# Performance work log

Measured on AMD Instinct MI355X. Metric: run time of the kernel, lower is better.

Reference implementation:

```python
import jax, jax.numpy as jnp
import numpy as np

S, D, BN, GH, AH, FCH = 18, 512, 32, 128, 16, 512


def setup_inputs() -> dict:
    key = jax.random.key(0)
    ks = jax.random.split(key, 20)
    B = 8192
    sc = 0.05
    inp = {
        "local_styles": jax.random.normal(ks[0], (B, S, D), jnp.float32),
        "global_styles": jax.random.normal(ks[1], (B, S, D), jnp.float32),
        "target_ages": jax.random.uniform(ks[2], (B,), jnp.float32),
        # per-style bottleneck MLPs (512->32->32), stacked over styles
        "bn_w1": jax.random.normal(ks[3], (S, D, BN), jnp.float32) * sc,
        "bn_b1": jnp.zeros((S, BN), jnp.float32),
        "bn_w2": jax.random.normal(ks[4], (S, BN, BN), jnp.float32) * sc,
        "bn_b2": jnp.zeros((S, BN), jnp.float32),
        # global mlp (18*32 -> 128 -> 128)
        "gm_w1": jax.random.normal(ks[5], (S * BN, GH), jnp.float32) * sc,
        "gm_b1": jnp.zeros((GH,), jnp.float32),
        "gm_w2": jax.random.normal(ks[6], (GH, GH), jnp.float32) * sc,
        "gm_b2": jnp.zeros((GH,), jnp.float32),
        # age mlp (1 -> 16 -> 16)
        "age_w1": jax.random.normal(ks[7], (1, AH), jnp.float32) * sc,
        "age_b1": jnp.zeros((AH,), jnp.float32),
        "age_w2": jax.random.normal(ks[8], (AH, AH), jnp.float32) * sc,
        "age_b2": jnp.zeros((AH,), jnp.float32),
        # per-style fc MLPs (128+16+512 -> 512 -> 512), stacked over styles
        "fc_w1": jax.random.normal(ks[9], (S, GH + AH + D, FCH), jnp.float32) * sc,
        "fc_b1": jnp.zeros((S, FCH), jnp.float32),
        "fc_w2": jax.random.normal(ks[10], (S, FCH, D), jnp.float32) * sc,
        "fc_b2": jnp.zeros((S, D), jnp.float32),
    }
    return inp


def reference(local_styles, global_styles, target_ages,
              bn_w1, bn_b1, bn_w2, bn_b2,
              gm_w1, gm_b1, gm_w2, gm_b2,
              age_w1, age_b1, age_w2, age_b2,
              fc_w1, fc_b1, fc_w2, fc_b2):
    B = global_styles.shape[0]
    # per-style bottlenecks as batched GEMMs over the style axis
    h = jax.nn.relu(jnp.einsum('bsd,sdk->bsk', global_styles, bn_w1) + bn_b1)
    h = jnp.einsum('bsk,skm->bsm', h, bn_w2) + bn_b2          # [B, S, 32]
    gf = h.reshape(B, S * BN)                                  # concat over styles
    gf = jax.nn.relu(gf @ gm_w1 + gm_b1) @ gm_w2 + gm_b2      # [B, 128]
    af = target_ages[:, None]                                  # [B, 1]
    af = jax.nn.relu(af @ age_w1 + age_b1) @ age_w2 + age_b2   # [B, 16]
    gfa = jnp.concatenate([gf, af], axis=1)                    # [B, 144]
    # per-style fc: input is [global_feats, style_i] -> [B, S, 656]
    x = jnp.concatenate([jnp.broadcast_to(gfa[:, None, :], (B, S, GH + AH)),
                         global_styles], axis=2)
    y = jax.nn.relu(jnp.einsum('bsf,sfh->bsh', x, fc_w1) + fc_b1)
    y = jnp.einsum('bsh,shd->bsd', y, fc_w2) + fc_b2
    return y + global_styles
```

## Files before the change

### kernel.cpp

```cpp
#include <hip/hip_runtime.h>

typedef unsigned short u16;
typedef unsigned int   u32;
typedef __attribute__((ext_vector_type(4))) float floatx4;
typedef __attribute__((ext_vector_type(8))) short shortx8;

#define BB 8192
#define SS 18
#define DD 512

__device__ __forceinline__ u16 f2bf(float f){
  u32 u = __float_as_uint(f);
  return (u16)((u + 0x7FFFu + ((u >> 16) & 1u)) >> 16);
}
__device__ __forceinline__ float bf2f(u16 x){ return __uint_as_float(((u32)x)<<16); }

__device__ __forceinline__ shortx8 pack8v(floatx4 a, floatx4 b){
  shortx8 t;
  t[0]=(short)f2bf(a[0]); t[1]=(short)f2bf(a[1]); t[2]=(short)f2bf(a[2]); t[3]=(short)f2bf(a[3]);
  t[4]=(short)f2bf(b[0]); t[5]=(short)f2bf(b[1]); t[6]=(short)f2bf(b[2]); t[7]=(short)f2bf(b[3]);
  return t;
}

__device__ __forceinline__ void gload16(const void* g, void* l){
  __builtin_amdgcn_global_load_lds((const __attribute__((address_space(1))) void*)g,
                                   (__attribute__((address_space(3))) void*)l, 16, 0, 0);
}

template<int CALLS>
__device__ __forceinline__ void gstage(const char* src, size_t rowStrideB, int chunkByteOff,
                                       char* lds, int wid, int lane){
#pragma unroll
  for (int i=0;i<CALLS;++i){
    int base = (wid*CALLS + i)*1024;
    int off  = base + lane*16;
    int row  = off >> 7;
    int blk  = ((off >> 4) & 7) ^ (row & 7);
    gload16(src + (size_t)row*rowStrideB + chunkByteOff + blk*16, lds + base);
  }
}

__device__ __forceinline__ void lds_store4(char* buf, int row, int rowBytes, int khByte,
                                           int swzMask, const shortx8* v){
#pragma unroll
  for (int q=0;q<4;++q){
    int off = row*rowBytes + khByte + q*16;
    off ^= (row & swzMask) << 4;
    *(shortx8*)(buf + off) = v[q];
  }
}

__device__ __forceinline__ void stage_bf16(char* buf, const u16* gsrc, size_t srcRowBytes, int tid){
  int row = tid >> 1, kh = tid & 1;
  const char* p = (const char*)gsrc + (size_t)row*srcRowBytes + kh*64;
  shortx8 v[4];
#pragma unroll
  for (int q=0;q<4;++q) v[q] = *(const shortx8*)(p + q*16);
  lds_store4(buf, row, 128, kh*64, 7, v);
}

__device__ __forceinline__ shortx8 lds_frag(const char* buf, int row, int rowBytes, int kByte,
                                            int swzMask, int lane){
  int off = row*rowBytes + kByte + ((lane>>4)<<4);
  off ^= (row & swzMask) << 4;
  return *(const shortx8*)(buf + off);
}

template<int MF, int NF>
__device__ __forceinline__ void mma64(const char* As, const char* Bs, int wm, int wn, int lane,
                                      floatx4 acc[MF][NF]){
#pragma unroll
  for (int kk=0; kk<2; ++kk){
    shortx8 a[MF], b[NF];
#pragma unroll
    for (int i=0;i<MF;++i) a[i] = lds_frag(As, wm + i*16 + (lane&15), 128, kk*64, 7, lane);
#pragma unroll
    for (int j=0;j<NF;++j) b[j] = lds_frag(Bs, wn + j*16 + (lane&15), 128, kk*64, 7, lane);
#pragma unroll
    for (int i=0;i<MF;++i)
#pragma unroll
      for (int j=0;j<NF;++j)
        acc[i][j] = __builtin_amdgcn_mfma_f32_16x16x32_bf16(a[i], b[j], acc[i][j], 0, 0, 0);
  }
}

template<int MF, int NF>
__device__ __forceinline__ void frags_load(const char* As, const char* Bs, int wm, int wn, int lane,
                                           shortx8 a[2][MF], shortx8 b[2][NF]){
#pragma unroll
  for (int kk=0;kk<2;++kk){
#pragma unroll
    for (int i=0;i<MF;++i) a[kk][i] = lds_frag(As, wm + i*16 + (lane&15), 128, kk*64, 7, lane);
#pragma unroll
    for (int j=0;j<NF;++j) b[kk][j] = lds_frag(Bs, wn + j*16 + (lane&15), 128, kk*64, 7, lane);
  }
}
template<int MF, int NF>
__device__ __forceinline__ void frags_mma(shortx8 a[2][MF], shortx8 b[2][NF], floatx4 acc[MF][NF]){
#pragma unroll
  for (int kk=0;kk<2;++kk)
#pragma unroll
    for (int i=0;i<MF;++i)
#pragma unroll
      for (int j=0;j<NF;++j)
        acc[i][j] = __builtin_amdgcn_mfma_f32_16x16x32_bf16(a[kk][i], b[kk][j], acc[i][j], 0, 0, 0);
}

__device__ __forceinline__ int xcd_swz(int bid, int nwg){
  int q = nwg >> 3;
  return (bid & 7)*q + (bid >> 3);
}

__global__ __launch_bounds__(256) void transpose_w2(const float* __restrict__ src,
                                                    u16* __restrict__ dst,
                                                    int sKstride, int kSrcOff, int Kuse,
                                                    int N, int Kpad, int kDstOff){
  __shared__ float tile[32][33];
  int s = blockIdx.z;
  int k0 = blockIdx.x*32, n0 = blockIdx.y*32;
  int tx = threadIdx.x & 31, ty = threadIdx.x >> 5;
#pragma unroll
  for (int r=0;r<4;++r){
    int k = k0 + ty*4 + r;
    float v = (k < Kuse) ? src[((size_t)s*sKstride + kSrcOff + k)*N + n0 + tx] : 0.f;
    tile[ty*4+r][tx] = v;
  }
  __syncthreads();
#pragma unroll
  for (int r=0;r<4;++r){
    int n = n0 + ty*4 + r;
    dst[((size_t)s*N + n)*Kpad + kDstOff + k0 + tx] = f2bf(tile[tx][ty*4+r]);
  }
}

__global__ __launch_bounds__(256) void k_bn(const float* __restrict__ gs,
     const u16* __restrict__ w1t, const u16* __restrict__ w2t,
     const float* __restrict__ b1, const float* __restrict__ b2,
     u16* __restrict__ h2b, u16* __restrict__ gsb){
  __shared__ __align__(16) char SMB[40960];
  int tid = threadIdx.x, lane = tid & 63, wid = tid >> 6;
  int nb = xcd_swz(blockIdx.x, 1152);
  int m0 = (nb & 63)*128, s = nb >> 6;
  floatx4 acc[2][2] = {};
  const char*  Bsrc = (const char*)w1t + (size_t)s*32*1024;
  size_t rowIdx = ((size_t)(m0 + (tid>>1))*SS + s)*DD + (tid&1)*32;
  const float* Ags  = gs + rowIdx;
  u16*         Gsb  = gsb + rowIdx;
  floatx4 fr[8];
  gstage<1>(Bsrc, 1024, 0, SMB+32768, wid, lane);
#pragma unroll
  for (int q=0;q<8;++q) fr[q] = *(const floatx4*)(Ags + q*4);
  for (int c=0;c<8;++c){
    char* Asc = SMB + (c&1)*16384;
    char* Bsc = SMB + 32768 + (c&1)*4096;
    { shortx8 v[4];
#pragma unroll
      for (int q=0;q<4;++q) v[q] = pack8v(fr[2*q], fr[2*q+1]);
      u16* gp = Gsb + c*64;
#pragma unroll
      for (int q=0;q<4;++q) *(shortx8*)(gp + q*8) = v[q];
      lds_store4(Asc, tid>>1, 128, (tid&1)*64, 7, v); }
    __syncthreads();
    int cn = c+1;
    if (cn < 8){
      gstage<1>(Bsrc, 1024, cn*128, SMB + 32768 + (cn&1)*4096, wid, lane);
      const float* p = Ags + cn*64;
#pragma unroll
      for (int q=0;q<8;++q) fr[q] = *(const floatx4*)(p + q*4);
    }
    mma64<2,2>(Asc, Bsc, wid*32, 0, lane, acc);
  }
  __syncthreads();
  char* G1  = SMB;
  char* W2s = SMB + 8192;
#pragma unroll
  for (int i=0;i<2;++i)
#pragma unroll
   for (int j=0;j<2;++j){
    int col = j*16 + (lane&15);
    float bias = b1[s*32 + col];
#pragma unroll
    for (int r=0;r<4;++r){
      int row = wid*32 + i*16 + ((lane>>4)<<2) + r;
      float v = fmaxf(acc[i][j][r] + bias, 0.f);
      int off = (row*64 + col*2) ^ ((row&3)<<4);
      *(u16*)(G1 + off) = f2bf(v);
    }
  }
  if (tid < 32){
    const u16* p = w2t + (size_t)s*32*32 + tid*32;
#pragma unroll
    for (int q=0;q<4;++q){
      int off = (tid*64 + q*16) ^ ((tid&3)<<4);
      *(shortx8*)(W2s + off) = *(const shortx8*)(p + q*8);
    }
  }
  __syncthreads();
  floatx4 acc2[2][2] = {};
  {
    shortx8 a[2], b[2];
#pragma unroll
    for (int i=0;i<2;++i) a[i] = lds_frag(G1,  wid*32 + i*16 + (lane&15), 64, 0, 3, lane);
#pragma unroll
    for (int j=0;j<2;++j) b[j] = lds_frag(W2s, j*16 + (lane&15),          64, 0, 3, lane);
#pragma unroll
    for (int i=0;i<2;++i)
#pragma unroll
      for (int j=0;j<2;++j)
        acc2[i][j] = __builtin_amdgcn_mfma_f32_16x16x32_bf16(a[i], b[j], acc2[i][j], 0,0,0);
  }
#pragma unroll
  for (int i=0;i<2;++i)
#pragma unroll
   for (int j=0;j<2;++j){
    int col = j*16 + (lane&15);
    float bias = b2[s*32 + col];
#pragma unroll
    for (int r=0;r<4;++r){
      int row = wid*32 + i*16 + ((lane>>4)<<2) + r;
      h2b[((size_t)(m0+row)*SS + s)*32 + col] = f2bf(acc2[i][j][r] + bias);
    }
  }
}

__global__ __launch_bounds__(256) void k_gm(const u16* __restrict__ h2b,
     const u16* __restrict__ w1t, const u16* __restrict__ w2t,
     const float* __restrict__ b1, const float* __restrict__ b2,
     const float* __restrict__ ta, const float* __restrict__ aw1, const float* __restrict__ ab1,
     const float* __restrict__ aw2, const float* __restrict__ ab2,
     u16* __restrict__ gfab){
  __shared__ __align__(16) char As[128*128];
  __shared__ __align__(16) char Bs[128*128];
  __shared__ __align__(16) char G1[128*256];
  int tid=threadIdx.x, lane=tid&63, w=tid>>6;
  int m0 = blockIdx.x*128;
  floatx4 acc[2][8] = {};
  for (int c=0;c<9;++c){
    __syncthreads();
    stage_bf16(As, h2b + (size_t)m0*576 + c*64, 1152, tid);
    stage_bf16(Bs, w1t + c*64,                 1152, tid);
    __syncthreads();
    mma64<2,8>(As, Bs, w*32, 0, lane, acc);
  }
#pragma unroll
  for (int i=0;i<2;++i)
#pragma unroll
   for (int j=0;j<8;++j){
    int col = j*16 + (lane&15);
    float bias = b1[col];
#pragma unroll
    for (int r=0;r<4;++r){
      int row = w*32 + i*16 + ((lane>>4)<<2) + r;
      float v = fmaxf(acc[i][j][r] + bias, 0.f);
      int off = (row*256 + col*2) ^ ((row&7)<<4);
      *(u16*)(G1 + off) = f2bf(v);
    }
  }
  floatx4 acc2[2][8] = {};
  for (int c2=0;c2<2;++c2){
    __syncthreads();
    stage_bf16(Bs, w2t + c2*64, 256, tid);
    __syncthreads();
#pragma unroll
    for (int kk=0;kk<2;++kk){
      shortx8 a[2], b[8];
#pragma unroll
      for (int i=0;i<2;++i){
        int row = w*32 + i*16 + (lane&15);
        int off = (row*256 + c2*128 + kk*64 + ((lane>>4)<<4)) ^ ((row&7)<<4);
        a[i] = *(const shortx8*)(G1 + off);
      }
#pragma unroll
      for (int j=0;j<8;++j) b[j] = lds_frag(Bs, j*16 + (lane&15), 128, kk*64, 7, lane);
#pragma unroll
      for (int i=0;i<2;++i)
#pragma unroll
        for (int j=0;j<8;++j)
          acc2[i][j] = __builtin_amdgcn_mfma_f32_16x16x32_bf16(a[i], b[j], acc2[i][j], 0,0,0);
    }
  }
#pragma unroll
  for (int i=0;i<2;++i)
#pragma unroll
   for (int j=0;j<8;++j){
    int col = j*16 + (lane&15);
    float bias = b2[col];
#pragma unroll
    for (int r=0;r<4;++r){
      int row = w*32 + i*16 + ((lane>>4)<<2) + r;
      gfab[(size_t)(m0+row)*192 + col] = f2bf(acc2[i][j][r] + bias);
    }
  }
  if (tid < 128){
    int bidx = m0 + tid;
    float t = ta[bidx];
    float a1[16];
#pragma unroll
    for (int j2=0;j2<16;++j2){ float v = t*aw1[j2] + ab1[j2]; a1[j2] = fmaxf(v, 0.f); }
#pragma unroll
    for (int m=0;m<16;++m){
      float v = ab2[m];
#pragma unroll
      for (int j2=0;j2<16;++j2) v += a1[j2]*aw2[j2*16+m];
      gfab[(size_t)bidx*192 + 128 + m] = f2bf(v);
    }
    shortx8 zz = {};
#pragma unroll
    for (int z=0;z<6;++z) *(shortx8*)(gfab + (size_t)bidx*192 + 144 + z*8) = zz;
  }
}

__global__ __launch_bounds__(256) void k_fc1(const u16* __restrict__ gfab,
     const u16* __restrict__ gsb, const u16* __restrict__ w1t,
     const float* __restrict__ b1, u16* __restrict__ y1b){
  __shared__ __align__(16) char SMB[81920];
  int tid=threadIdx.x, lane=tid&63, wid=tid>>6;
  int nb = xcd_swz(blockIdx.x, 4608);
  int n0=(nb&3)*128, m0=((nb>>2)&63)*128, s=nb>>8;
  int wm=(wid>>1)*64, wn=(wid&1)*64;
  floatx4 acc[4][4] = {};
  const char* Ag   = (const char*)gfab + (size_t)m0*384;
  const char* Agl  = (const char*)gsb + ((size_t)m0*SS + s)*1024;
  const char* Bsrc = (const char*)w1t + ((size_t)s*512+n0)*1408;
#define F1_ISSA(t) do{ int _t=(t); char* _d = SMB + (_t%3)*16384; \
    if (_t<3) gstage<4>(Ag, 384, _t*128, _d, wid, lane); \
    else      gstage<4>(Agl, (size_t)SS*1024, _t*128-384, _d, wid, lane); }while(0)
#define F1_ISSB(t) gstage<4>(Bsrc, 1408, (t)*128, SMB+49152+((t)&1)*16384, wid, lane)
  F1_ISSB(0); F1_ISSA(0); F1_ISSA(1);
#pragma unroll 1
  for (int c=0;c<11;++c){
    if (c<10) asm volatile("s_waitcnt vmcnt(4)" ::: "memory");
    else      asm volatile("s_waitcnt vmcnt(0)" ::: "memory");
    __builtin_amdgcn_s_barrier();
    __builtin_amdgcn_sched_barrier(0);
    shortx8 a[2][4], b[2][4];
    frags_load<4,4>(SMB+(c%3)*16384, SMB+49152+(c&1)*16384, wm, wn, lane, a, b);
    if (c+1<11) F1_ISSB(c+1);
    if (c+2<11) F1_ISSA(c+2);
    frags_mma<4,4>(a, b, acc);
  }
  __syncthreads();
  char* OT = SMB;
#pragma unroll
  for (int i=0;i<4;++i)
#pragma unroll
   for (int j=0;j<4;++j){
    int col = wn + j*16 + (lane&15);
    float bias = b1[(size_t)s*512 + n0 + col];
#pragma unroll
    for (int r=0;r<4;++r){
      int row = wm + i*16 + ((lane>>4)<<2) + r;
      float v = fmaxf(acc[i][j][r] + bias, 0.f);
      int off = (row*256 + col*2) ^ ((row&7)<<4);
      *(u16*)(OT + off) = f2bf(v);
    }
  }
  __syncthreads();
  {
    int row = tid>>1, half = tid&1;
    u16* gp = y1b + ((size_t)(m0+row)*SS + s)*DD + n0 + half*64;
#pragma unroll
    for (int q=0;q<8;++q){
      int off = (row*256 + half*128 + q*16) ^ ((row&7)<<4);
      *(shortx8*)(gp + q*8) = *(const shortx8*)(OT + off);
    }
  }
}

__global__ __launch_bounds__(256) void k_fc2(const u16* __restrict__ y1b,
     const u16* __restrict__ gsb, const u16* __restrict__ w2t,
     const float* __restrict__ b2, float* __restrict__ out){
  __shared__ __align__(16) char SMB[81920];
  int tid=threadIdx.x, lane=tid&63, wid=tid>>6;
  int nb = xcd_swz(blockIdx.x, 4608);
  int n0=(nb&3)*128, m0=((nb>>2)&63)*128, s=nb>>8;
  int wm=(wid>>1)*64, wn=(wid&1)*64;
  floatx4 acc[4][4] = {};
  const char* Asrc = (const char*)y1b + ((size_t)m0*SS + s)*1024;
  const char* Bsrc = (const char*)w2t + ((size_t)s*512 + n0)*1024;
#define F2_ISSA(t) gstage<4>(Asrc, (size_t)SS*1024, (t)*128, SMB+((t)%3)*16384, wid, lane)
#define F2_ISSB(t) gstage<4>(Bsrc, 1024, (t)*128, SMB+49152+((t)&1)*16384, wid, lane)
  F2_ISSB(0); F2_ISSA(0); F2_ISSA(1);
#pragma unroll 1
  for (int c=0;c<8;++c){
    if (c<7) asm volatile("s_waitcnt vmcnt(4)" ::: "memory");
    else     asm volatile("s_waitcnt vmcnt(0)" ::: "memory");
    __builtin_amdgcn_s_barrier();
    __builtin_amdgcn_sched_barrier(0);
    shortx8 a[2][4], b[2][4];
    frags_load<4,4>(SMB+(c%3)*16384, SMB+49152+(c&1)*16384, wm, wn, lane, a, b);
    if (c+1<8) F2_ISSB(c+1);
    if (c+2<8) F2_ISSA(c+2);
    frags_mma<4,4>(a, b, acc);
  }
  __syncthreads();
  float* SMF = (float*)SMB;
#pragma unroll
  for (int i=0;i<4;++i)
#pragma unroll
   for (int j=0;j<4;++j){
    int col = wn + j*16 + (lane&15);
#pragma unroll
    for (int r=0;r<4;++r){
      int row = wm + i*16 + ((lane>>4)<<2) + r;
      int off = (row*512 + col*4) ^ ((row&7)<<4);
      *(float*)((char*)SMF + off) = acc[i][j][r];
    }
  }
  __syncthreads();
  {
    int row = tid>>1, half = tid&1;
    size_t gidx = ((size_t)(m0+row)*SS + s)*DD + n0 + half*64;
    const float* bp = b2 + (size_t)s*512 + n0 + half*64;
    const u16*   gp = gsb + gidx;
#pragma unroll
    for (int q2=0;q2<8;++q2){
      shortx8 gv = *(const shortx8*)(gp + q2*8);
      int off0 = (row*512 + half*256 + (2*q2)*16)   ^ ((row&7)<<4);
      int off1 = (row*512 + half*256 + (2*q2+1)*16) ^ ((row&7)<<4);
      floatx4 v0 = *(const floatx4*)((char*)SMF + off0);
      floatx4 v1 = *(const floatx4*)((char*)SMF + off1);
      floatx4 b0 = *(const floatx4*)(bp + q2*8);
      floatx4 b1v= *(const floatx4*)(bp + q2*8 + 4);
      floatx4 g0, g1;
      g0[0]=bf2f((u16)gv[0]); g0[1]=bf2f((u16)gv[1]); g0[2]=bf2f((u16)gv[2]); g0[3]=bf2f((u16)gv[3]);
      g1[0]=bf2f((u16)gv[4]); g1[1]=bf2f((u16)gv[5]); g1[2]=bf2f((u16)gv[6]); g1[3]=bf2f((u16)gv[7]);
      *(floatx4*)(out + gidx + q2*8)     = v0 + b0 + g0;
      *(floatx4*)(out + gidx + q2*8 + 4) = v1 + b1v + g1;
    }
  }
}

extern "C" void kernel_launch(void* const* d_in, const int* in_sizes, int n_in,
                              void* d_out, int out_size, void* d_ws, size_t ws_size,
                              hipStream_t stream){
  (void)in_sizes; (void)n_in; (void)out_size; (void)ws_size;
  const float* gs   = (const float*)d_in[1];
  const float* ta   = (const float*)d_in[2];
  const float* bnw1 = (const float*)d_in[3];
  const float* bnb1 = (const float*)d_in[4];
  const float* bnw2 = (const float*)d_in[5];
  const float* bnb2 = (const float*)d_in[6];
  const float* gmw1 = (const float*)d_in[7];
  const float* gmb1 = (const float*)d_in[8];
  const float* gmw2 = (const float*)d_in[9];
  const float* gmb2 = (const float*)d_in[10];
  const float* aw1  = (const float*)d_in[11];
  const float* ab1  = (const float*)d_in[12];
  const float* aw2  = (const float*)d_in[13];
  const float* ab2  = (const float*)d_in[14];
  const float* fcw1 = (const float*)d_in[15];
  const float* fcb1 = (const float*)d_in[16];
  const float* fcw2 = (const float*)d_in[17];
  const float* fcb2 = (const float*)d_in[18];

  char* ws = (char*)d_ws;
  u16* fcW1t = (u16*)(ws + 0);
  u16* fcW2t = (u16*)(ws + 12976128);
  u16* bnW1t = (u16*)(ws + 22413312);
  u16* bnW2t = (u16*)(ws + 23003136);
  u16* gmW1t = (u16*)(ws + 23040000);
  u16* gmW2t = (u16*)(ws + 23187456);
  u16* h2b   = (u16*)(ws + 23220224);
  u16* gfab  = (u16*)(ws + 32657408);
  u16* y1b   = (u16*)(ws + 35803136);
  u16* gsb   = (u16*)(ws + 186798080);
  float* out = (float*)d_out;

  dim3 blk(256);
  transpose_w2<<<dim3(16,1,18),  blk, 0, stream>>>(bnw1, bnW1t, 512, 0, 512,  32, 512, 0);
  transpose_w2<<<dim3(1,1,18),   blk, 0, stream>>>(bnw2, bnW2t,  32, 0,  32,  32,  32, 0);
  transpose_w2<<<dim3(18,4,1),   blk, 0, stream>>>(gmw1, gmW1t, 576, 0, 576, 128, 576, 0);
  transpose_w2<<<dim3(4,4,1),    blk, 0, stream>>>(gmw2, gmW2t, 128, 0, 128, 128, 128, 0);
  transpose_w2<<<dim3(6,16,18),  blk, 0, stream>>>(fcw1, fcW1t, 656, 0,   144, 512, 704, 0);
  transpose_w2<<<dim3(16,16,18), blk, 0, stream>>>(fcw1, fcW1t, 656, 144, 512, 512, 704, 192);
  transpose_w2<<<dim3(16,16,18), blk, 0, stream>>>(fcw2, fcW2t, 512, 0, 512, 512, 512, 0);

  k_bn <<<dim3(1152), blk, 0, stream>>>(gs, bnW1t, bnW2t, bnb1, bnb2, h2b, gsb);
  k_gm <<<dim3(64),   blk, 0, stream>>>(h2b, gmW1t, gmW2t, gmb1, gmb2, ta, aw1, ab1, aw2, ab2, gfab);
  k_fc1<<<dim3(4608), blk, 0, stream>>>(gfab, gsb, fcW1t, fcb1, y1b);
  k_fc2<<<dim3(4608), blk, 0, stream>>>(y1b, gsb, fcW2t, fcb2, out);
}
```

Measured before the change: 573.4 us.

## Enlarge fc GEMM tiles to 256x256 with 512-thread blocks and double buffering

Both per-style fc GEMM kernels move from 128x128 tiles with 256 threads to 256x256 tiles with 512 threads (8 waves, each holding a 128x64 accumulator). LDS staging changes from a triple-buffered A / double-buffered B scheme to plain double buffering, with an extra barrier before refilling. MFMA issue is wrapped in s_setprio. The goal is more operand reuse per byte loaded and fewer blocks. In exchange, LDS use is 128 KB and each thread holds more accumulator registers, which limits occupancy to one block per CU. The fc2 epilogue is split into two halves so the fp32 tile fits in shared memory.

```diff
diff --git a/kernel.cpp b/kernel.cpp
--- a/kernel.cpp
+++ b/kernel.cpp
@@ -40,6 +40,23 @@
   }
 }
 
+__device__ __forceinline__ void gstage8(const char* src, size_t rowStrideB, int chunkByteOff,
+                                        char* lds, int wid, int lane){
+#pragma unroll
+  for (int i=0;i<2;++i){
+    int base = (wid*2 + i)*1024;
+    int off  = base + lane*16;
+    int row  = off >> 7;
+    int blk  = ((off >> 4) & 7) ^ (row & 7);
+    gload16(src + (size_t)row*rowStrideB + chunkByteOff + blk*16, lds + base);
+  }
+}
+__device__ __forceinline__ void stage256(const char* src, size_t rowStrideB, int chunkByteOff,
+                                         char* lds, int wid, int lane){
+  gstage8(src, rowStrideB, chunkByteOff, lds, wid, lane);
+  gstage8(src + 128*rowStrideB, rowStrideB, chunkByteOff, lds + 16384, wid, lane);
+}
+
 __device__ __forceinline__ void lds_store4(char* buf, int row, int rowBytes, int khByte,
                                            int swzMask, const shortx8* v){
 #pragma unroll
@@ -84,26 +101,23 @@
   }
 }
 
-template<int MF, int NF>
-__device__ __forceinline__ void frags_load(const char* As, const char* Bs, int wm, int wn, int lane,
-                                           shortx8 a[2][MF], shortx8 b[2][NF]){
+__device__ __forceinline__ void mma_256tile(const char* Ab, const char* Bb, int wm, int wn,
+                                            int lane, floatx4 acc[8][4]){
 #pragma unroll
   for (int kk=0;kk<2;++kk){
-#pragma unroll
-    for (int i=0;i<MF;++i) a[kk][i] = lds_frag(As, wm + i*16 + (lane&15), 128, kk*64, 7, lane);
-#pragma unroll
-    for (int j=0;j<NF;++j) b[kk][j] = lds_frag(Bs, wn + j*16 + (lane&15), 128, kk*64, 7, lane);
-  }
-}
-template<int MF, int NF>
-__device__ __forceinline__ void frags_mma(shortx8 a[2][MF], shortx8 b[2][NF], floatx4 acc[MF][NF]){
-#pragma unroll
-  for (int kk=0;kk<2;++kk)
-#pragma unroll
-    for (int i=0;i<MF;++i)
-#pragma unroll
-      for (int j=0;j<NF;++j)
-        acc[i][j] = __builtin_amdgcn_mfma_f32_16x16x32_bf16(a[kk][i], b[kk][j], acc[i][j], 0, 0, 0);
+    shortx8 a[8], b[4];
+#pragma unroll
+    for (int i=0;i<8;++i) a[i] = lds_frag(Ab, wm + i*16 + (lane&15), 128, kk*64, 7, lane);
+#pragma unroll
+    for (int j=0;j<4;++j) b[j] = lds_frag(Bb, wn + j*16 + (lane&15), 128, kk*64, 7, lane);
+    __builtin_amdgcn_s_setprio(1);
+#pragma unroll
+    for (int i=0;i<8;++i)
+#pragma unroll
+      for (int j=0;j<4;++j)
+        acc[i][j] = __builtin_amdgcn_mfma_f32_16x16x32_bf16(a[i], b[j], acc[i][j], 0, 0, 0);
+    __builtin_amdgcn_s_setprio(0);
+  }
 }
 
 __device__ __forceinline__ int xcd_swz(int bid, int nwg){
@@ -310,123 +324,132 @@
   }
 }
 
-__global__ __launch_bounds__(256) void k_fc1(const u16* __restrict__ gfab,
+__global__ __launch_bounds__(512) void k_fc1(const u16* __restrict__ gfab,
      const u16* __restrict__ gsb, const u16* __restrict__ w1t,
      const float* __restrict__ b1, u16* __restrict__ y1b){
-  __shared__ __align__(16) char SMB[81920];
+  __shared__ __align__(16) char SMB[131072];
   int tid=threadIdx.x, lane=tid&63, wid=tid>>6;
-  int nb = xcd_swz(blockIdx.x, 4608);
-  int n0=(nb&3)*128, m0=((nb>>2)&63)*128, s=nb>>8;
-  int wm=(wid>>1)*64, wn=(wid&1)*64;
-  floatx4 acc[4][4] = {};
-  const char* Ag   = (const char*)gfab + (size_t)m0*384;
-  const char* Agl  = (const char*)gsb + ((size_t)m0*SS + s)*1024;
-  const char* Bsrc = (const char*)w1t + ((size_t)s*512+n0)*1408;
-#define F1_ISSA(t) do{ int _t=(t); char* _d = SMB + (_t%3)*16384; \
-    if (_t<3) gstage<4>(Ag, 384, _t*128, _d, wid, lane); \
-    else      gstage<4>(Agl, (size_t)SS*1024, _t*128-384, _d, wid, lane); }while(0)
-#define F1_ISSB(t) gstage<4>(Bsrc, 1408, (t)*128, SMB+49152+((t)&1)*16384, wid, lane)
-  F1_ISSB(0); F1_ISSA(0); F1_ISSA(1);
+  int nb = xcd_swz(blockIdx.x, 1152);
+  int n1 = nb&1, m0 = ((nb>>1)&31)*256, s = nb>>6;
+  int wm = (wid>>2)*128, wn = (wid&3)*64;
+  floatx4 acc[8][4] = {};
+  const char* A0 = (const char*)gfab + (size_t)m0*384;
+  const char* A1 = (const char*)gsb + ((size_t)m0*SS + s)*1024;
+  const char* Bb = (const char*)w1t + ((size_t)s*512 + n1*256)*1408;
+#define C1_ISSA(t) do{ int _t=(t); char* _d = SMB + (_t&1)*32768; \
+    if (_t<3) stage256(A0, 384, _t*128, _d, wid, lane); \
+    else      stage256(A1, (size_t)SS*1024, _t*128-384, _d, wid, lane); }while(0)
+#define C1_ISSB(t) stage256(Bb, 1408, (t)*128, SMB + 65536 + ((t)&1)*32768, wid, lane)
+  C1_ISSA(0); C1_ISSB(0); C1_ISSA(1); C1_ISSB(1);
 #pragma unroll 1
   for (int c=0;c<11;++c){
-    if (c<10) asm volatile("s_waitcnt vmcnt(4)" ::: "memory");
+    if (c<10) asm volatile("s_waitcnt vmcnt(8)" ::: "memory");
     else      asm volatile("s_waitcnt vmcnt(0)" ::: "memory");
     __builtin_amdgcn_s_barrier();
     __builtin_amdgcn_sched_barrier(0);
-    shortx8 a[2][4], b[2][4];
-    frags_load<4,4>(SMB+(c%3)*16384, SMB+49152+(c&1)*16384, wm, wn, lane, a, b);
-    if (c+1<11) F1_ISSB(c+1);
-    if (c+2<11) F1_ISSA(c+2);
-    frags_mma<4,4>(a, b, acc);
+    const char* Ab = SMB + (c&1)*32768;
+    const char* Bbuf = SMB + 65536 + (c&1)*32768;
+    mma_256tile(Ab, Bbuf, wm, wn, lane, acc);
+    asm volatile("s_waitcnt lgkmcnt(0)" ::: "memory");
+    __builtin_amdgcn_s_barrier();
+    __builtin_amdgcn_sched_barrier(0);
+    if (c+2<11){ C1_ISSA(c+2); C1_ISSB(c+2); }
   }
   __syncthreads();
-  char* OT = SMB;
-#pragma unroll
-  for (int i=0;i<4;++i)
+#pragma unroll
+  for (int i=0;i<8;++i)
 #pragma unroll
    for (int j=0;j<4;++j){
     int col = wn + j*16 + (lane&15);
-    float bias = b1[(size_t)s*512 + n0 + col];
+    float bias = b1[(size_t)s*512 + n1*256 + col];
 #pragma unroll
     for (int r=0;r<4;++r){
       int row = wm + i*16 + ((lane>>4)<<2) + r;
       float v = fmaxf(acc[i][j][r] + bias, 0.f);
-      int off = (row*256 + col*2) ^ ((row&7)<<4);
-      *(u16*)(OT + off) = f2bf(v);
+      int off = (row*512 + col*2) ^ ((row&7)<<4);
+      *(u16*)(SMB + off) = f2bf(v);
     }
   }
   __syncthreads();
   {
     int row = tid>>1, half = tid&1;
-    u16* gp = y1b + ((size_t)(m0+row)*SS + s)*DD + n0 + half*64;
-#pragma unroll
-    for (int q=0;q<8;++q){
-      int off = (row*256 + half*128 + q*16) ^ ((row&7)<<4);
-      *(shortx8*)(gp + q*8) = *(const shortx8*)(OT + off);
-    }
-  }
-}
-
-__global__ __launch_bounds__(256) void k_fc2(const u16* __restrict__ y1b,
+    u16* gp = y1b + ((size_t)(m0+row)*SS + s)*DD + n1*256 + half*128;
+#pragma unroll
+    for (int q=0;q<16;++q){
+      int off = (row*512 + half*256 + q*16) ^ ((row&7)<<4);
+      *(shortx8*)(gp + q*8) = *(const shortx8*)(SMB + off);
+    }
+  }
+}
+
+__global__ __launch_bounds__(512) void k_fc2(const u16* __restrict__ y1b,
      const u16* __restrict__ gsb, const u16* __restrict__ w2t,
      const float* __restrict__ b2, float* __restrict__ out){
-  __shared__ __align__(16) char SMB[81920];
+  __shared__ __align__(16) char SMB[131072];
   int tid=threadIdx.x, lane=tid&63, wid=tid>>6;
-  int nb = xcd_swz(blockIdx.x, 4608);
-  int n0=(nb&3)*128, m0=((nb>>2)&63)*128, s=nb>>8;
-  int wm=(wid>>1)*64, wn=(wid&1)*64;
-  floatx4 acc[4][4] = {};
-  const char* Asrc = (const char*)y1b + ((size_t)m0*SS + s)*1024;
-  const char* Bsrc = (const char*)w2t + ((size_t)s*512 + n0)*1024;
-#define F2_ISSA(t) gstage<4>(Asrc, (size_t)SS*1024, (t)*128, SMB+((t)%3)*16384, wid, lane)
-#define F2_ISSB(t) gstage<4>(Bsrc, 1024, (t)*128, SMB+49152+((t)&1)*16384, wid, lane)
-  F2_ISSB(0); F2_ISSA(0); F2_ISSA(1);
+  int nb = xcd_swz(blockIdx.x, 1152);
+  int n1 = nb&1, m0 = ((nb>>1)&31)*256, s = nb>>6;
+  int wm = (wid>>2)*128, wn = (wid&3)*64;
+  floatx4 acc[8][4] = {};
+  const char* Ab0 = (const char*)y1b + ((size_t)m0*SS + s)*1024;
+  const char* Bb  = (const char*)w2t + ((size_t)s*512 + n1*256)*1024;
+#define C2_ISSA(t) stage256(Ab0, (size_t)SS*1024, (t)*128, SMB + ((t)&1)*32768, wid, lane)
+#define C2_ISSB(t) stage256(Bb, 1024, (t)*128, SMB + 65536 + ((t)&1)*32768, wid, lane)
+  C2_ISSA(0); C2_ISSB(0); C2_ISSA(1); C2_ISSB(1);
 #pragma unroll 1
   for (int c=0;c<8;++c){
-    if (c<7) asm volatile("s_waitcnt vmcnt(4)" ::: "memory");
+    if (c<7) asm volatile("s_waitcnt vmcnt(8)" ::: "memory");
     else     asm volatile("s_waitcnt vmcnt(0)" ::: "memory");
     __builtin_amdgcn_s_barrier();
     __builtin_amdgcn_sched_barrier(0);
-    shortx8 a[2][4], b[2][4];
-    frags_load<4,4>(SMB+(c%3)*16384, SMB+49152+(c&1)*16384, wm, wn, lane, a, b);
-    if (c+1<8) F2_ISSB(c+1);
-    if (c+2<8) F2_ISSA(c+2);
-    frags_mma<4,4>(a, b, acc);
-  }
-  __syncthreads();
+    const char* Ab = SMB + (c&1)*32768;
+    const char* Bbuf = SMB + 65536 + (c&1)*32768;
+    mma_256tile(Ab, Bbuf, wm, wn, lane, acc);
+    asm volatile("s_waitcnt lgkmcnt(0)" ::: "memory");
+    __builtin_amdgcn_s_barrier();
+    __builtin_amdgcn_sched_barrier(0);
+    if (c+2<8){ C2_ISSA(c+2); C2_ISSB(c+2); }
+  }
   float* SMF = (float*)SMB;
-#pragma unroll
-  for (int i=0;i<4;++i)
-#pragma unroll
-   for (int j=0;j<4;++j){
-    int col = wn + j*16 + (lane&15);
-#pragma unroll
-    for (int r=0;r<4;++r){
-      int row = wm + i*16 + ((lane>>4)<<2) + r;
-      int off = (row*512 + col*4) ^ ((row&7)<<4);
-      *(float*)((char*)SMF + off) = acc[i][j][r];
-    }
-  }
-  __syncthreads();
-  {
-    int row = tid>>1, half = tid&1;
-    size_t gidx = ((size_t)(m0+row)*SS + s)*DD + n0 + half*64;
-    const float* bp = b2 + (size_t)s*512 + n0 + half*64;
-    const u16*   gp = gsb + gidx;
-#pragma unroll
-    for (int q2=0;q2<8;++q2){
-      shortx8 gv = *(const shortx8*)(gp + q2*8);
-      int off0 = (row*512 + half*256 + (2*q2)*16)   ^ ((row&7)<<4);
-      int off1 = (row*512 + half*256 + (2*q2+1)*16) ^ ((row&7)<<4);
-      floatx4 v0 = *(const floatx4*)((char*)SMF + off0);
-      floatx4 v1 = *(const floatx4*)((char*)SMF + off1);
-      floatx4 b0 = *(const floatx4*)(bp + q2*8);
-      floatx4 b1v= *(const floatx4*)(bp + q2*8 + 4);
-      floatx4 g0, g1;
-      g0[0]=bf2f((u16)gv[0]); g0[1]=bf2f((u16)gv[1]); g0[2]=bf2f((u16)gv[2]); g0[3]=bf2f((u16)gv[3]);
-      g1[0]=bf2f((u16)gv[4]); g1[1]=bf2f((u16)gv[5]); g1[2]=bf2f((u16)gv[6]); g1[3]=bf2f((u16)gv[7]);
-      *(floatx4*)(out + gidx + q2*8)     = v0 + b0 + g0;
-      *(floatx4*)(out + gidx + q2*8 + 4) = v1 + b1v + g1;
+#pragma unroll 1
+  for (int h=0;h<2;++h){
+    __syncthreads();
+    if ((wid>>2) == h){
+#pragma unroll
+      for (int i=0;i<8;++i)
+#pragma unroll
+       for (int j=0;j<4;++j){
+        int col = wn + j*16 + (lane&15);
+#pragma unroll
+        for (int r=0;r<4;++r){
+          int rl = i*16 + ((lane>>4)<<2) + r;
+          int off = (rl*1024 + col*4) ^ ((rl&7)<<4);
+          *(float*)((char*)SMF + off) = acc[i][j][r];
+        }
+      }
+    }
+    __syncthreads();
+    {
+      int rl = tid>>2, quarter = tid&3;
+      int grow = m0 + h*128 + rl;
+      size_t gidx = ((size_t)grow*SS + s)*DD + n1*256 + quarter*64;
+      const float* bp = b2 + (size_t)s*512 + n1*256 + quarter*64;
+      const u16*   gp = gsb + gidx;
+#pragma unroll
+      for (int q2=0;q2<8;++q2){
+        shortx8 gv = *(const shortx8*)(gp + q2*8);
+        int off0 = (rl*1024 + quarter*256 + q2*32)      ^ ((rl&7)<<4);
+        int off1 = (rl*1024 + quarter*256 + q2*32 + 16) ^ ((rl&7)<<4);
+        floatx4 v0 = *(const floatx4*)((char*)SMF + off0);
+        floatx4 v1 = *(const floatx4*)((char*)SMF + off1);
+        floatx4 b0 = *(const floatx4*)(bp + q2*8);
+        floatx4 b1v= *(const floatx4*)(bp + q2*8 + 4);
+        floatx4 g0, g1;
+        g0[0]=bf2f((u16)gv[0]); g0[1]=bf2f((u16)gv[1]); g0[2]=bf2f((u16)gv[2]); g0[3]=bf2f((u16)gv[3]);
+        g1[0]=bf2f((u16)gv[4]); g1[1]=bf2f((u16)gv[5]); g1[2]=bf2f((u16)gv[6]); g1[3]=bf2f((u16)gv[7]);
+        *(floatx4*)(out + gidx + q2*8)     = v0 + b0 + g0;
+        *(floatx4*)(out + gidx + q2*8 + 4) = v1 + b1v + g1;
+      }
     }
   }
 }
@@ -476,8 +499,8 @@
   transpose_w2<<<dim3(16,16,18), blk, 0, stream>>>(fcw1, fcW1t, 656, 144, 512, 512, 704, 192);
   transpose_w2<<<dim3(16,16,18), blk, 0, stream>>>(fcw2, fcW2t, 512, 0, 512, 512, 512, 0);
 
-  k_bn <<<dim3(1152), blk, 0, stream>>>(gs, bnW1t, bnW2t, bnb1, bnb2, h2b, gsb);
-  k_gm <<<dim3(64),   blk, 0, stream>>>(h2b, gmW1t, gmW2t, gmb1, gmb2, ta, aw1, ab1, aw2, ab2, gfab);
-  k_fc1<<<dim3(4608), blk, 0, stream>>>(gfab, gsb, fcW1t, fcb1, y1b);
-  k_fc2<<<dim3(4608), blk, 0, stream>>>(y1b, gsb, fcW2t, fcb2, out);
-}
+  k_bn <<<dim3(1152), blk,      0, stream>>>(gs, bnW1t, bnW2t, bnb1, bnb2, h2b, gsb);
+  k_gm <<<dim3(64),   blk,      0, stream>>>(h2b, gmW1t, gmW2t, gmb1, gmb2, ta, aw1, ab1, aw2, ab2, gfab);
+  k_fc1<<<dim3(1152), dim3(512), 0, stream>>>(gfab, gsb, fcW1t, fcb1, y1b);
+  k_fc2<<<dim3(1152), dim3(512), 0, stream>>>(y1b, gsb, fcW2t, fcb2, out);
+}
```

Result: slower. 910.3 us (+58.7%).

## Widen FC GEMM tiles to 128x256 with 512-thread blocks and register-staged A

Applied to the files above, without the earlier changes.

The fc1 and fc2 GEMM kernels now use 512-thread blocks, each computing a 128x256 output tile, which halves the grid size and increases reuse of the A operand per block. A tiles are prefetched into registers three chunks ahead and written to double-buffered LDS, while B tiles are loaded straight into triple-buffered LDS. The MFMA sections are wrapped in raised wave priority. The fc2 epilogue is split into two halves so it fits the LDS layout. Each block now needs 128KB of LDS and more registers, which limits occupancy to about one block per CU and adds more manual waitcnt bookkeeping.

```diff
diff --git a/kernel.cpp b/kernel.cpp
--- a/kernel.cpp
+++ b/kernel.cpp
@@ -97,6 +97,7 @@
 }
 template<int MF, int NF>
 __device__ __forceinline__ void frags_mma(shortx8 a[2][MF], shortx8 b[2][NF], floatx4 acc[MF][NF]){
+  __builtin_amdgcn_s_setprio(1);
 #pragma unroll
   for (int kk=0;kk<2;++kk)
 #pragma unroll
@@ -104,6 +105,7 @@
 #pragma unroll
       for (int j=0;j<NF;++j)
         acc[i][j] = __builtin_amdgcn_mfma_f32_16x16x32_bf16(a[kk][i], b[kk][j], acc[i][j], 0, 0, 0);
+  __builtin_amdgcn_s_setprio(0);
 }
 
 __device__ __forceinline__ int xcd_swz(int bid, int nwg){
@@ -310,123 +312,175 @@
   }
 }
 
-__global__ __launch_bounds__(256) void k_fc1(const u16* __restrict__ gfab,
+__global__ __launch_bounds__(512, 2) void k_fc1(const u16* __restrict__ gfab,
      const u16* __restrict__ gsb, const u16* __restrict__ w1t,
      const float* __restrict__ b1, u16* __restrict__ y1b){
-  __shared__ __align__(16) char SMB[81920];
+  __shared__ __align__(16) char SMB[131072];
   int tid=threadIdx.x, lane=tid&63, wid=tid>>6;
-  int nb = xcd_swz(blockIdx.x, 4608);
-  int n0=(nb&3)*128, m0=((nb>>2)&63)*128, s=nb>>8;
-  int wm=(wid>>1)*64, wn=(wid&1)*64;
+  int nb = xcd_swz(blockIdx.x, 2304);
+  int n1 = nb&1, m0 = ((nb>>1)&63)*128, s = nb>>7;
+  int wm = (wid>>2)*64, wn = (wid&3)*64;
   floatx4 acc[4][4] = {};
-  const char* Ag   = (const char*)gfab + (size_t)m0*384;
-  const char* Agl  = (const char*)gsb + ((size_t)m0*SS + s)*1024;
-  const char* Bsrc = (const char*)w1t + ((size_t)s*512+n0)*1408;
-#define F1_ISSA(t) do{ int _t=(t); char* _d = SMB + (_t%3)*16384; \
-    if (_t<3) gstage<4>(Ag, 384, _t*128, _d, wid, lane); \
-    else      gstage<4>(Agl, (size_t)SS*1024, _t*128-384, _d, wid, lane); }while(0)
-#define F1_ISSB(t) gstage<4>(Bsrc, 1408, (t)*128, SMB+49152+((t)&1)*16384, wid, lane)
-  F1_ISSB(0); F1_ISSA(0); F1_ISSA(1);
-#pragma unroll 1
+  int ar = tid>>2, aq = (tid&3)*32;
+  const char* pAg = (const char*)gfab + (size_t)(m0+ar)*384 + aq;
+  const char* pAs = (const char*)gsb + ((size_t)(m0+ar)*SS + s)*1024 + aq;
+  int wo0 = ar*128 + ( aq      ^ ((ar&7)<<4));
+  int wo1 = ar*128 + ((aq+16)  ^ ((ar&7)<<4));
+  const char* gW = (const char*)w1t + ((size_t)s*512 + n1*256)*1408;
+  const char* pB[4]; int ldB[4];
+#pragma unroll
+  for (int i=0;i<4;++i){
+    int base=(wid*4+i)*1024, off=base+lane*16;
+    int row=off>>7, blk=((off>>4)&7)^(row&7);
+    pB[i] = gW + (size_t)row*1408 + blk*16;
+    ldB[i] = base;
+  }
+  floatx4 qA0[2], qA1[2], qA2[2];
+#define QS1(c) ((c)%3==0?qA0:((c)%3==1?qA1:qA2))
+#define LDA1(c,Q) do{ if((c)<3){ Q[0]=*(const floatx4*)(pAg+(c)*128); Q[1]=*(const floatx4*)(pAg+(c)*128+16); } \
+                      else     { Q[0]=*(const floatx4*)(pAs+((c)-3)*128); Q[1]=*(const floatx4*)(pAs+((c)-3)*128+16); } }while(0)
+#define ISSB1(c) do{ char* _d=SMB+32768+((c)%3)*32768; \
+    gload16(pB[0]+(c)*128,_d+ldB[0]); gload16(pB[1]+(c)*128,_d+ldB[1]); \
+    gload16(pB[2]+(c)*128,_d+ldB[2]); gload16(pB[3]+(c)*128,_d+ldB[3]); }while(0)
+  LDA1(0,qA0); __builtin_amdgcn_sched_barrier(0);
+  ISSB1(0);    __builtin_amdgcn_sched_barrier(0);
+  LDA1(1,qA1); __builtin_amdgcn_sched_barrier(0);
+  ISSB1(1);    __builtin_amdgcn_sched_barrier(0);
+  LDA1(2,qA2); __builtin_amdgcn_sched_barrier(0);
+#pragma unroll
   for (int c=0;c<11;++c){
-    if (c<10) asm volatile("s_waitcnt vmcnt(4)" ::: "memory");
-    else      asm volatile("s_waitcnt vmcnt(0)" ::: "memory");
+    if (c<9)       asm volatile("s_waitcnt vmcnt(8)" ::: "memory");
+    else if (c==9) asm volatile("s_waitcnt vmcnt(6)" ::: "memory");
+    else           asm volatile("s_waitcnt vmcnt(0)" ::: "memory");
+    { char* As = SMB + (c&1)*16384;
+      const floatx4* Q = QS1(c);
+      *(floatx4*)(As+wo0) = Q[0]; *(floatx4*)(As+wo1) = Q[1]; }
+    asm volatile("s_waitcnt lgkmcnt(0)" ::: "memory");
     __builtin_amdgcn_s_barrier();
+    shortx8 a[2][4], b[2][4];
+    frags_load<4,4>(SMB + (c&1)*16384, SMB + 32768 + (c%3)*32768, wm, wn, lane, a, b);
     __builtin_amdgcn_sched_barrier(0);
-    shortx8 a[2][4], b[2][4];
-    frags_load<4,4>(SMB+(c%3)*16384, SMB+49152+(c&1)*16384, wm, wn, lane, a, b);
-    if (c+1<11) F1_ISSB(c+1);
-    if (c+2<11) F1_ISSA(c+2);
+    if (c+2<11) ISSB1(c+2);
+    if (c+3<11) { LDA1(c+3, QS1(c+3)); }
+    __builtin_amdgcn_sched_barrier(0);
     frags_mma<4,4>(a, b, acc);
   }
   __syncthreads();
-  char* OT = SMB;
 #pragma unroll
   for (int i=0;i<4;++i)
 #pragma unroll
    for (int j=0;j<4;++j){
     int col = wn + j*16 + (lane&15);
-    float bias = b1[(size_t)s*512 + n0 + col];
+    float bias = b1[(size_t)s*512 + n1*256 + col];
 #pragma unroll
     for (int r=0;r<4;++r){
       int row = wm + i*16 + ((lane>>4)<<2) + r;
       float v = fmaxf(acc[i][j][r] + bias, 0.f);
-      int off = (row*256 + col*2) ^ ((row&7)<<4);
-      *(u16*)(OT + off) = f2bf(v);
+      int off = (row*512 + col*2) ^ ((row&7)<<4);
+      *(u16*)(SMB + off) = f2bf(v);
     }
   }
   __syncthreads();
   {
-    int row = tid>>1, half = tid&1;
-    u16* gp = y1b + ((size_t)(m0+row)*SS + s)*DD + n0 + half*64;
+    int row = tid>>2, cq = tid&3;
+    u16* gp = y1b + ((size_t)(m0+row)*SS + s)*DD + n1*256 + cq*64;
 #pragma unroll
     for (int q=0;q<8;++q){
-      int off = (row*256 + half*128 + q*16) ^ ((row&7)<<4);
-      *(shortx8*)(gp + q*8) = *(const shortx8*)(OT + off);
-    }
-  }
-}
-
-__global__ __launch_bounds__(256) void k_fc2(const u16* __restrict__ y1b,
+      int off = (row*512 + cq*128 + q*16) ^ ((row&7)<<4);
+      *(shortx8*)(gp + q*8) = *(const shortx8*)(SMB + off);
+    }
+  }
+}
+
+__global__ __launch_bounds__(512, 2) void k_fc2(const u16* __restrict__ y1b,
      const u16* __restrict__ gsb, const u16* __restrict__ w2t,
      const float* __restrict__ b2, float* __restrict__ out){
-  __shared__ __align__(16) char SMB[81920];
+  __shared__ __align__(16) char SMB[131072];
   int tid=threadIdx.x, lane=tid&63, wid=tid>>6;
-  int nb = xcd_swz(blockIdx.x, 4608);
-  int n0=(nb&3)*128, m0=((nb>>2)&63)*128, s=nb>>8;
-  int wm=(wid>>1)*64, wn=(wid&1)*64;
+  int nb = xcd_swz(blockIdx.x, 2304);
+  int n1 = nb&1, m0 = ((nb>>1)&63)*128, s = nb>>7;
+  int wm = (wid>>2)*64, wn = (wid&3)*64;
   floatx4 acc[4][4] = {};
-  const char* Asrc = (const char*)y1b + ((size_t)m0*SS + s)*1024;
-  const char* Bsrc = (const char*)w2t + ((size_t)s*512 + n0)*1024;
-#define F2_ISSA(t) gstage<4>(Asrc, (size_t)SS*1024, (t)*128, SMB+((t)%3)*16384, wid, lane)
-#define F2_ISSB(t) gstage<4>(Bsrc, 1024, (t)*128, SMB+49152+((t)&1)*16384, wid, lane)
-  F2_ISSB(0); F2_ISSA(0); F2_ISSA(1);
+  int ar = tid>>2, aq = (tid&3)*32;
+  const char* pA = (const char*)y1b + ((size_t)(m0+ar)*SS + s)*1024 + aq;
+  int wo0 = ar*128 + ( aq      ^ ((ar&7)<<4));
+  int wo1 = ar*128 + ((aq+16)  ^ ((ar&7)<<4));
+  const char* gW = (const char*)w2t + ((size_t)s*512 + n1*256)*1024;
+  const char* pB[4]; int ldB[4];
+#pragma unroll
+  for (int i=0;i<4;++i){
+    int base=(wid*4+i)*1024, off=base+lane*16;
+    int row=off>>7, blk=((off>>4)&7)^(row&7);
+    pB[i] = gW + (size_t)row*1024 + blk*16;
+    ldB[i] = base;
+  }
+  floatx4 qA0[2], qA1[2], qA2[2];
+#define QS2(c) ((c)%3==0?qA0:((c)%3==1?qA1:qA2))
+#define LDA2(c,Q) do{ Q[0]=*(const floatx4*)(pA+(c)*128); Q[1]=*(const floatx4*)(pA+(c)*128+16); }while(0)
+#define ISSB2(c) do{ char* _d=SMB+32768+((c)%3)*32768; \
+    gload16(pB[0]+(c)*128,_d+ldB[0]); gload16(pB[1]+(c)*128,_d+ldB[1]); \
+    gload16(pB[2]+(c)*128,_d+ldB[2]); gload16(pB[3]+(c)*128,_d+ldB[3]); }while(0)
+  LDA2(0,qA0); __builtin_amdgcn_sched_barrier(0);
+  ISSB2(0);    __builtin_amdgcn_sched_barrier(0);
+  LDA2(1,qA1); __builtin_amdgcn_sched_barrier(0);
+  ISSB2(1);    __builtin_amdgcn_sched_barrier(0);
+  LDA2(2,qA2); __builtin_amdgcn_sched_barrier(0);
+#pragma unroll
+  for (int c=0;c<8;++c){
+    if (c<6)       asm volatile("s_waitcnt vmcnt(8)" ::: "memory");
+    else if (c==6) asm volatile("s_waitcnt vmcnt(6)" ::: "memory");
+    else           asm volatile("s_waitcnt vmcnt(0)" ::: "memory");
+    { char* As = SMB + (c&1)*16384;
+      const floatx4* Q = QS2(c);
+      *(floatx4*)(As+wo0) = Q[0]; *(floatx4*)(As+wo1) = Q[1]; }
+    asm volatile("s_waitcnt lgkmcnt(0)" ::: "memory");
+    __builtin_amdgcn_s_barrier();
+    shortx8 a[2][4], b[2][4];
+    frags_load<4,4>(SMB + (c&1)*16384, SMB + 32768 + (c%3)*32768, wm, wn, lane, a, b);
+    __builtin_amdgcn_sched_barrier(0);
+    if (c+2<8) ISSB2(c+2);
+    if (c+3<8) { LDA2(c+3, QS2(c+3)); }
+    __builtin_amdgcn_sched_barrier(0);
+    frags_mma<4,4>(a, b, acc);
+  }
+  float* SMF = (float*)SMB;
 #pragma unroll 1
-  for (int c=0;c<8;++c){
-    if (c<7) asm volatile("s_waitcnt vmcnt(4)" ::: "memory");
-    else     asm volatile("s_waitcnt vmcnt(0)" ::: "memory");
-    __builtin_amdgcn_s_barrier();
-    __builtin_amdgcn_sched_barrier(0);
-    shortx8 a[2][4], b[2][4];
-    frags_load<4,4>(SMB+(c%3)*16384, SMB+49152+(c&1)*16384, wm, wn, lane, a, b);
-    if (c+1<8) F2_ISSB(c+1);
-    if (c+2<8) F2_ISSA(c+2);
-    frags_mma<4,4>(a, b, acc);
-  }
-  __syncthreads();
-  float* SMF = (float*)SMB;
-#pragma unroll
-  for (int i=0;i<4;++i)
-#pragma unroll
-   for (int j=0;j<4;++j){
-    int col = wn + j*16 + (lane&15);
-#pragma unroll
-    for (int r=0;r<4;++r){
-      int row = wm + i*16 + ((lane>>4)<<2) + r;
-      int off = (row*512 + col*4) ^ ((row&7)<<4);
-      *(float*)((char*)SMF + off) = acc[i][j][r];
-    }
-  }
-  __syncthreads();
-  {
-    int row = tid>>1, half = tid&1;
-    size_t gidx = ((size_t)(m0+row)*SS + s)*DD + n0 + half*64;
-    const float* bp = b2 + (size_t)s*512 + n0 + half*64;
-    const u16*   gp = gsb + gidx;
-#pragma unroll
-    for (int q2=0;q2<8;++q2){
-      shortx8 gv = *(const shortx8*)(gp + q2*8);
-      int off0 = (row*512 + half*256 + (2*q2)*16)   ^ ((row&7)<<4);
-      int off1 = (row*512 + half*256 + (2*q2+1)*16) ^ ((row&7)<<4);
-      floatx4 v0 = *(const floatx4*)((char*)SMF + off0);
-      floatx4 v1 = *(const floatx4*)((char*)SMF + off1);
-      floatx4 b0 = *(const floatx4*)(bp + q2*8);
-      floatx4 b1v= *(const floatx4*)(bp + q2*8 + 4);
-      floatx4 g0, g1;
-      g0[0]=bf2f((u16)gv[0]); g0[1]=bf2f((u16)gv[1]); g0[2]=bf2f((u16)gv[2]); g0[3]=bf2f((u16)gv[3]);
-      g1[0]=bf2f((u16)gv[4]); g1[1]=bf2f((u16)gv[5]); g1[2]=bf2f((u16)gv[6]); g1[3]=bf2f((u16)gv[7]);
-      *(floatx4*)(out + gidx + q2*8)     = v0 + b0 + g0;
-      *(floatx4*)(out + gidx + q2*8 + 4) = v1 + b1v + g1;
+  for (int h=0;h<2;++h){
+    __syncthreads();
+    if ((wid>>2) == h){
+#pragma unroll
+      for (int i=0;i<4;++i)
+#pragma unroll
+       for (int j=0;j<4;++j){
+        int col = wn + j*16 + (lane&15);
+#pragma unroll
+        for (int r=0;r<4;++r){
+          int rl = i*16 + ((lane>>4)<<2) + r;
+          int off = (rl*1024 + col*4) ^ ((rl&7)<<4);
+          *(float*)((char*)SMF + off) = acc[i][j][r];
+        }
+      }
+    }
+    __syncthreads();
+    {
+      int rl = tid>>3, c8 = tid&7;
+      int grow = m0 + h*64 + rl;
+      size_t gidx = ((size_t)grow*SS + s)*DD + n1*256 + c8*32;
+      const float* bp = b2 + (size_t)s*512 + n1*256 + c8*32;
+      const u16*   gp = gsb + gidx;
+      shortx8 gv[4];
+#pragma unroll
+      for (int q=0;q<4;++q) gv[q] = *(const shortx8*)(gp + q*8);
+#pragma unroll
+      for (int q=0;q<8;++q){
+        int off = (rl*1024 + c8*128 + q*16) ^ ((rl&7)<<4);
+        floatx4 v = *(const floatx4*)((char*)SMF + off);
+        floatx4 bb = *(const floatx4*)(bp + q*4);
+        floatx4 g;
+        g[0]=bf2f((u16)gv[q>>1][(q&1)*4+0]); g[1]=bf2f((u16)gv[q>>1][(q&1)*4+1]);
+        g[2]=bf2f((u16)gv[q>>1][(q&1)*4+2]); g[3]=bf2f((u16)gv[q>>1][(q&1)*4+3]);
+        *(floatx4*)(out + gidx + q*4) = v + bb + g;
+      }
     }
   }
 }
@@ -476,8 +530,8 @@
   transpose_w2<<<dim3(16,16,18), blk, 0, stream>>>(fcw1, fcW1t, 656, 144, 512, 512, 704, 192);
   transpose_w2<<<dim3(16,16,18), blk, 0, stream>>>(fcw2, fcW2t, 512, 0, 512, 512, 512, 0);
 
-  k_bn <<<dim3(1152), blk, 0, stream>>>(gs, bnW1t, bnW2t, bnb1, bnb2, h2b, gsb);
-  k_gm <<<dim3(64),   blk, 0, stream>>>(h2b, gmW1t, gmW2t, gmb1, gmb2, ta, aw1, ab1, aw2, ab2, gfab);
-  k_fc1<<<dim3(4608), blk, 0, stream>>>(gfab, gsb, fcW1t, fcb1, y1b);
-  k_fc2<<<dim3(4608), blk, 0, stream>>>(y1b, gsb, fcW2t, fcb2, out);
-}
+  k_bn <<<dim3(1152), blk,       0, stream>>>(gs, bnW1t, bnW2t, bnb1, bnb2, h2b, gsb);
+  k_gm <<<dim3(64),   blk,       0, stream>>>(h2b, gmW1t, gmW2t, gmb1, gmb2, ta, aw1, ab1, aw2, ab2, gfab);
+  k_fc1<<<dim3(2304), dim3(512), 0, stream>>>(gfab, gsb, fcW1t, fcb1, y1b);
+  k_fc2<<<dim3(2304), dim3(512), 0, stream>>>(y1b, gsb, fcW2t, fcb2, out);
+}
```

After: 609.3 us. +6.3%, slower.
